# Kernel optimization log

Measured on AMD Instinct MI355X. Metric: run time of the kernel, lower is better.

The kernel has to match this reference:

```python
import jax, jax.numpy as jnp
import numpy as np

N_NODES = 100000
IN_CH, HIDDEN, OUT_CH = 128, 128, 64
N_POS, N_NEG = 600000, 600000


def _glorot(key, shape):
    lim = float(np.sqrt(6.0 / (shape[0] + shape[1])))
    return jax.random.uniform(key, shape, jnp.float32, -lim, lim)


def setup_inputs() -> dict:
    key = jax.random.key(0)
    k = jax.random.split(key, 7)
    x = jax.random.normal(k[0], (N_NODES, IN_CH), jnp.float32)
    pos_edge_index = jax.random.randint(k[1], (2, N_POS), 0, N_NODES, jnp.int64)
    neg_edge_index = jax.random.randint(k[2], (2, N_NEG), 0, N_NODES, jnp.int64)
    W1 = _glorot(k[3], (IN_CH, HIDDEN))
    b1 = jnp.zeros((HIDDEN,), jnp.float32)
    W2 = _glorot(k[4], (HIDDEN, OUT_CH))
    b2 = jnp.zeros((OUT_CH,), jnp.float32)
    return {"x": x, "pos_edge_index": pos_edge_index, "neg_edge_index": neg_edge_index,
            "W1": W1, "b1": b1, "W2": W2, "b2": b2}


def gcn_conv(x, W, b, src, dst, n_nodes):
    # PyG GCNConv: add self-loops, symmetric deg^-1/2 normalization, linear, bias
    h = x @ W                                               # [N, F_out]
    ones = jnp.ones(src.shape, h.dtype)
    deg = jax.ops.segment_sum(ones, dst, num_segments=n_nodes) + 1.0  # self-loop
    dinv = jax.lax.rsqrt(deg)                               # deg^-0.5, deg >= 1
    norm = dinv[src] * dinv[dst]                            # per-edge norm
    agg = jax.ops.segment_sum(h[src] * norm[:, None], dst, num_segments=n_nodes)
    agg = agg + h * (dinv * dinv)[:, None]                  # self-loop messages
    return agg + b


def reference(x, pos_edge_index, neg_edge_index, W1, b1, W2, b2):
    n = x.shape[0]
    src, dst = pos_edge_index[0], pos_edge_index[1]
    z = gcn_conv(x, W1, b1, src, dst, n)
    z = jax.nn.relu(z)
    z = gcn_conv(z, W2, b2, src, dst, n)
    # decode: gather endpoints of pos+neg edges, elementwise product, sum over feat
    ei = jnp.concatenate([pos_edge_index, neg_edge_index], axis=-1)  # [2, E_pos+E_neg]
    return jnp.sum(z[ei[0]] * z[ei[1]], axis=-1)
```

## Files before the change

### kernel.cpp

```cpp
#include <hip/hip_runtime.h>

#define N_NODES 100000
#define IN_CH 128
#define HIDDEN 128
#define OUT_CH 64
#define N_POS 600000
#define N_NEG 600000

typedef unsigned int uint32;
typedef unsigned short ushort16;
typedef __attribute__((ext_vector_type(8))) short bf16x8;
typedef __attribute__((ext_vector_type(4))) float f32x4;

__device__ inline float bf_lo(uint32 u) {
    union { uint32 i; float f; } v;
    v.i = u << 16;
    return v.f;
}
__device__ inline float bf_hi(uint32 u) {
    union { uint32 i; float f; } v;
    v.i = u & 0xffff0000u;
    return v.f;
}
__device__ inline ushort16 f2bf(float f) {
    union { uint32 i; float f; } v;
    v.f = f;
    uint32 r = v.i + 0x7fffu + ((v.i >> 16) & 1u);
    return (ushort16)(r >> 16);
}
__device__ inline uint32 pack2bf(float a, float b) {
    return (uint32)f2bf(a) | ((uint32)f2bf(b) << 16);
}

#define NB_HIST4 ((N_POS / 4 + 255) / 256)
#define NB_FILL4 ((N_POS / 4 + 255) / 256)
#define NB_GEMM1 ((N_NODES + 63) / 64)

__global__ void hist_wt(const int* __restrict__ dst, int* __restrict__ hist,
                        const float* __restrict__ W1, const float* __restrict__ W2,
                        ushort16* __restrict__ W1t, ushort16* __restrict__ W2t) {
    if (blockIdx.x < NB_HIST4) {
        int e = (blockIdx.x * 256 + threadIdx.x) * 4;
        if (e < N_POS) {
            int4 d4 = *(const int4*)(dst + e);
            atomicAdd(&hist[d4.x], 1);
            atomicAdd(&hist[d4.y], 1);
            atomicAdd(&hist[d4.z], 1);
            atomicAdd(&hist[d4.w], 1);
        }
    } else {
        int i = (blockIdx.x - NB_HIST4) * 256 + threadIdx.x;
        if (i < 128 * 128) {
            int n = i >> 7, k = i & 127;
            W1t[i] = f2bf(W1[k * 128 + n]);
        } else {
            int j = i - 128 * 128;
            if (j < 64 * 128) {
                int n = j >> 7, k = j & 127;
                W2t[j] = f2bf(W2[k * 64 + n]);
            }
        }
    }
}

__global__ void scan_reduce(const int* __restrict__ hist, int* __restrict__ partials, int n) {
    __shared__ int sdata[256];
    int b = blockIdx.x, t = threadIdx.x;
    int base = b * 1024;
    int s = 0;
    for (int i = t; i < 1024; i += 256) {
        int idx = base + i;
        s += (idx < n) ? hist[idx] : 0;
    }
    sdata[t] = s;
    __syncthreads();
    for (int off = 128; off > 0; off >>= 1) {
        if (t < off) sdata[t] += sdata[t + off];
        __syncthreads();
    }
    if (t == 0) partials[b] = sdata[0];
}

__global__ void scan_final(const int* __restrict__ hist, const int* __restrict__ partials,
                           int* __restrict__ rowstart, int* __restrict__ cursor,
                           float* __restrict__ dinv, int n) {
    __shared__ int tsum[256];
    __shared__ int base_sh;
    int t = threadIdx.x, b = blockIdx.x;
    if (t < 64) {
        int s0 = (t < b) ? partials[t] : 0;
        int i2 = t + 64;
        int s1 = (i2 < b && i2 < 98) ? partials[i2] : 0;
        int s = s0 + s1;
#pragma unroll
        for (int off = 32; off > 0; off >>= 1) s += __shfl_down(s, off, 64);
        if (t == 0) base_sh = s;
    }
    int base = b * 1024 + t * 4;
    int v[4];
    int s = 0;
#pragma unroll
    for (int j = 0; j < 4; j++) {
        int i = base + j;
        v[j] = (i < n) ? hist[i] : 0;
        s += v[j];
    }
    tsum[t] = s;
    __syncthreads();
    for (int off = 1; off < 256; off <<= 1) {
        int a = (t >= off) ? tsum[t - off] : 0;
        __syncthreads();
        tsum[t] += a;
        __syncthreads();
    }
    int offset = base_sh + (tsum[t] - s);
#pragma unroll
    for (int j = 0; j < 4; j++) {
        int i = base + j;
        if (i < n) {
            rowstart[i] = offset;
            cursor[i] = offset;
            dinv[i] = rsqrtf((float)v[j] + 1.0f);
            offset += v[j];
        }
    }
    if (b == 0 && t == 0) rowstart[n] = N_POS;
}

template <int M, bool XBF>
__device__ __forceinline__ void gemm_tile(const void* __restrict__ Xv,
                                          const ushort16* __restrict__ Wt,
                                          ushort16* __restrict__ H, int n, int tileIdx) {
    constexpr int K = 128;
    constexpr int TN = 64;
    constexpr int KH = 64;
    constexpr int XS = 72;
    __shared__ short Xs[TN * XS];
    __shared__ short Ws[M * XS];
    int tid = threadIdx.x;
    int node0 = tileIdx * TN;

    constexpr int CT = M / 16;
    int w = tid >> 6;
    int lane = tid & 63;
    int l15 = lane & 15;
    int quad = lane >> 4;
    f32x4 acc[CT] = {};

#pragma unroll
    for (int h = 0; h < 2; ++h) {
        if (h) __syncthreads();
        for (int q = tid; q < M * 8; q += 256) {
            int row = q >> 3, c = q & 7;
            uint4 v = *(const uint4*)((const short*)Wt + row * K + h * KH + c * 8);
            *(uint4*)(Ws + row * XS + c * 8) = v;
        }
        if (!XBF) {
            const float* X = (const float*)Xv;
            int row = tid >> 2, part = tid & 3;
            int gn = node0 + row;
#pragma unroll
            for (int c = 0; c < 4; ++c) {
                int kl = part * 16 + c * 4;
                float4 v = (gn < n) ? *(const float4*)(X + (size_t)gn * K + h * KH + kl)
                                    : float4{0, 0, 0, 0};
                uint2 p = {pack2bf(v.x, v.y), pack2bf(v.z, v.w)};
                *(uint2*)(Xs + row * XS + kl) = p;
            }
        } else {
            const short* X = (const short*)Xv;
            for (int q = tid; q < TN * 8; q += 256) {
                int row = q >> 3, c = q & 7;
                int gn = node0 + row;
                uint4 v = (gn < n) ? *(const uint4*)(X + (size_t)gn * K + h * KH + c * 8)
                                   : uint4{0, 0, 0, 0};
                *(uint4*)(Xs + row * XS + c * 8) = v;
            }
        }
        __syncthreads();

        const short* xrow = Xs + (w * 16 + l15) * XS + quad * 8;
#pragma unroll
        for (int kk = 0; kk < 2; ++kk) {
            bf16x8 a = *(const bf16x8*)(xrow + kk * 32);
#pragma unroll
            for (int ct = 0; ct < CT; ++ct) {
                bf16x8 b = *(const bf16x8*)(Ws + (ct * 16 + l15) * XS + quad * 8 + kk * 32);
                acc[ct] = __builtin_amdgcn_mfma_f32_16x16x32_bf16(a, b, acc[ct], 0, 0, 0);
            }
        }
    }

#pragma unroll
    for (int ct = 0; ct < CT; ++ct) {
#pragma unroll
        for (int r = 0; r < 4; ++r) {
            int gn = node0 + w * 16 + quad * 4 + r;
            if (gn < n) H[(size_t)gn * M + ct * 16 + l15] = f2bf(acc[ct][r]);
        }
    }
}

__global__ __launch_bounds__(256) void csr_gemm1(
    const int* __restrict__ src, const int* __restrict__ dst, const float* __restrict__ dinv,
    int* __restrict__ cursor, int2* __restrict__ adjw, const float* __restrict__ x,
    const ushort16* __restrict__ W1t, ushort16* __restrict__ H, int n) {
    if (blockIdx.x < NB_FILL4) {
        int e = (blockIdx.x * 256 + threadIdx.x) * 4;
        if (e < N_POS) {
            int4 s4 = *(const int4*)(src + e);
            int4 d4 = *(const int4*)(dst + e);
            float a0 = dinv[s4.x], a1 = dinv[s4.y], a2 = dinv[s4.z], a3 = dinv[s4.w];
            float c0 = dinv[d4.x], c1 = dinv[d4.y], c2 = dinv[d4.z], c3 = dinv[d4.w];
            int p0 = atomicAdd(&cursor[d4.x], 1);
            int p1 = atomicAdd(&cursor[d4.y], 1);
            int p2 = atomicAdd(&cursor[d4.z], 1);
            int p3 = atomicAdd(&cursor[d4.w], 1);
            adjw[p0] = int2{s4.x, __float_as_int(a0 * c0)};
            adjw[p1] = int2{s4.y, __float_as_int(a1 * c1)};
            adjw[p2] = int2{s4.z, __float_as_int(a2 * c2)};
            adjw[p3] = int2{s4.w, __float_as_int(a3 * c3)};
        }
    } else {
        gemm_tile<HIDDEN, false>(x, W1t, H, n, blockIdx.x - NB_FILL4);
    }
}

__device__ __forceinline__ uint4 agg_node128(int node, int l, const int* __restrict__ rowstart,
                                             const int2* __restrict__ adjw,
                                             const float* __restrict__ dinv,
                                             const ushort16* __restrict__ H,
                                             const float* __restrict__ bias) {
    float dn = dinv[node];
    int rs = rowstart[node], re = rowstart[node + 1];
    int deg = re - rs;
    int pc = (deg > 0) ? rs : (rs > 0 ? rs - 1 : 0);
    uint4 h[8];
    float wv[8];
#pragma unroll
    for (int j = 0; j < 8; ++j) {
        int p = (rs + j < re) ? rs + j : pc;
        int2 e = adjw[p];
        h[j] = *(const uint4*)(H + (size_t)e.x * 128 + l * 8);
        wv[j] = (j < deg) ? __int_as_float(e.y) : 0.0f;
    }
    float s0[8] = {}, s1[8] = {};
#pragma unroll
    for (int j = 0; j < 8; j += 2) {
        s0[0] += bf_lo(h[j].x) * wv[j]; s0[1] += bf_hi(h[j].x) * wv[j];
        s0[2] += bf_lo(h[j].y) * wv[j]; s0[3] += bf_hi(h[j].y) * wv[j];
        s0[4] += bf_lo(h[j].z) * wv[j]; s0[5] += bf_hi(h[j].z) * wv[j];
        s0[6] += bf_lo(h[j].w) * wv[j]; s0[7] += bf_hi(h[j].w) * wv[j];
        s1[0] += bf_lo(h[j + 1].x) * wv[j + 1]; s1[1] += bf_hi(h[j + 1].x) * wv[j + 1];
        s1[2] += bf_lo(h[j + 1].y) * wv[j + 1]; s1[3] += bf_hi(h[j + 1].y) * wv[j + 1];
        s1[4] += bf_lo(h[j + 1].z) * wv[j + 1]; s1[5] += bf_hi(h[j + 1].z) * wv[j + 1];
        s1[6] += bf_lo(h[j + 1].w) * wv[j + 1]; s1[7] += bf_hi(h[j + 1].w) * wv[j + 1];
    }
    for (int p = rs + 8; p < re; ++p) {
        int2 e = adjw[p];
        float w = __int_as_float(e.y);
        uint4 hh = *(const uint4*)(H + (size_t)e.x * 128 + l * 8);
        s0[0] += bf_lo(hh.x) * w; s0[1] += bf_hi(hh.x) * w;
        s0[2] += bf_lo(hh.y) * w; s0[3] += bf_hi(hh.y) * w;
        s0[4] += bf_lo(hh.z) * w; s0[5] += bf_hi(hh.z) * w;
        s0[6] += bf_lo(hh.w) * w; s0[7] += bf_hi(hh.w) * w;
    }
    uint4 hv = *(const uint4*)(H + (size_t)node * 128 + l * 8);
    float4 bv0 = *(const float4*)(bias + l * 8);
    float4 bv1 = *(const float4*)(bias + l * 8 + 4);
    float d2 = dn * dn;
    float hs[8] = {bf_lo(hv.x), bf_hi(hv.x), bf_lo(hv.y), bf_hi(hv.y),
                   bf_lo(hv.z), bf_hi(hv.z), bf_lo(hv.w), bf_hi(hv.w)};
    float bb[8] = {bv0.x, bv0.y, bv0.z, bv0.w, bv1.x, bv1.y, bv1.z, bv1.w};
    float v[8];
#pragma unroll
    for (int j = 0; j < 8; ++j) {
        v[j] = fmaxf(s0[j] + s1[j] + hs[j] * d2 + bb[j], 0.0f);
    }
    return uint4{pack2bf(v[0], v[1]), pack2bf(v[2], v[3]), pack2bf(v[4], v[5]),
                 pack2bf(v[6], v[7])};
}

#define ZS 136
__global__ __launch_bounds__(256, 4) void agg1_gemm2(
    const int* __restrict__ rowstart, const int2* __restrict__ adjw,
    const float* __restrict__ dinv, const ushort16* __restrict__ H,
    const float* __restrict__ b1, const ushort16* __restrict__ W2t,
    ushort16* __restrict__ h2, int n) {
    __shared__ __align__(16) short Zs[64 * ZS];
    __shared__ __align__(16) short Ws[64 * ZS];
    int tid = threadIdx.x;
    int node0 = blockIdx.x * 64;

    for (int q = tid; q < 64 * 16; q += 256) {
        int row = q >> 4, c = q & 15;
        uint4 v = *(const uint4*)((const short*)W2t + row * 128 + c * 8);
        *(uint4*)(Ws + row * ZS + c * 8) = v;
    }

    int g = tid >> 4, l = tid & 15;
#pragma unroll 1
    for (int it = 0; it < 4; ++it) {
        int row = g * 4 + it;
        int node = node0 + row;
        uint4 z = (node < n) ? agg_node128(node, l, rowstart, adjw, dinv, H, b1)
                             : uint4{0, 0, 0, 0};
        *(uint4*)(Zs + row * ZS + l * 8) = z;
    }
    __syncthreads();

    int w = tid >> 6, lane = tid & 63, l15 = lane & 15, quad = lane >> 4;
    f32x4 acc[4] = {};
    const short* zrow = Zs + (w * 16 + l15) * ZS + quad * 8;
#pragma unroll
    for (int kk = 0; kk < 4; ++kk) {
        bf16x8 a = *(const bf16x8*)(zrow + kk * 32);
#pragma unroll
        for (int ct = 0; ct < 4; ++ct) {
            bf16x8 b = *(const bf16x8*)(Ws + (ct * 16 + l15) * ZS + quad * 8 + kk * 32);
            acc[ct] = __builtin_amdgcn_mfma_f32_16x16x32_bf16(a, b, acc[ct], 0, 0, 0);
        }
    }
#pragma unroll
    for (int ct = 0; ct < 4; ++ct) {
#pragma unroll
        for (int r = 0; r < 4; ++r) {
            int gn = node0 + w * 16 + quad * 4 + r;
            if (gn < n) h2[(size_t)gn * OUT_CH + ct * 16 + l15] = f2bf(acc[ct][r]);
        }
    }
}

template <int F, bool RELU>
__global__ void agg_pull(const int* __restrict__ rowstart, const int2* __restrict__ adjw,
                         const float* __restrict__ dinv, const ushort16* __restrict__ H,
                         const float* __restrict__ bias, ushort16* __restrict__ Z, int n) {
    int g = threadIdx.x >> 4;
    int l = threadIdx.x & 15;
    int node = blockIdx.x * (blockDim.x >> 4) + g;
    if (node >= n) return;
    float dn = dinv[node];
    int rs = rowstart[node], re = rowstart[node + 1];
    int deg = re - rs;
    int pc = (deg > 0) ? rs : (rs > 0 ? rs - 1 : 0);
    if (F == 128) {
        uint4 h[8];
        float wv[8];
#pragma unroll
        for (int j = 0; j < 8; ++j) {
            int p = (rs + j < re) ? rs + j : pc;
            int2 e = adjw[p];
            h[j] = *(const uint4*)(H + (size_t)e.x * F + l * 8);
            wv[j] = (j < deg) ? __int_as_float(e.y) : 0.0f;
        }
        float s0[8] = {}, s1[8] = {};
#pragma unroll
        for (int j = 0; j < 8; j += 2) {
            s0[0] += bf_lo(h[j].x) * wv[j]; s0[1] += bf_hi(h[j].x) * wv[j];
            s0[2] += bf_lo(h[j].y) * wv[j]; s0[3] += bf_hi(h[j].y) * wv[j];
            s0[4] += bf_lo(h[j].z) * wv[j]; s0[5] += bf_hi(h[j].z) * wv[j];
            s0[6] += bf_lo(h[j].w) * wv[j]; s0[7] += bf_hi(h[j].w) * wv[j];
            s1[0] += bf_lo(h[j + 1].x) * wv[j + 1]; s1[1] += bf_hi(h[j + 1].x) * wv[j + 1];
            s1[2] += bf_lo(h[j + 1].y) * wv[j + 1]; s1[3] += bf_hi(h[j + 1].y) * wv[j + 1];
            s1[4] += bf_lo(h[j + 1].z) * wv[j + 1]; s1[5] += bf_hi(h[j + 1].z) * wv[j + 1];
            s1[6] += bf_lo(h[j + 1].w) * wv[j + 1]; s1[7] += bf_hi(h[j + 1].w) * wv[j + 1];
        }
        for (int p = rs + 8; p < re; ++p) {
            int2 e = adjw[p];
            float w = __int_as_float(e.y);
            uint4 hh = *(const uint4*)(H + (size_t)e.x * F + l * 8);
            s0[0] += bf_lo(hh.x) * w; s0[1] += bf_hi(hh.x) * w;
            s0[2] += bf_lo(hh.y) * w; s0[3] += bf_hi(hh.y) * w;
            s0[4] += bf_lo(hh.z) * w; s0[5] += bf_hi(hh.z) * w;
            s0[6] += bf_lo(hh.w) * w; s0[7] += bf_hi(hh.w) * w;
        }
        uint4 hv = *(const uint4*)(H + (size_t)node * F + l * 8);
        float4 bv0 = *(const float4*)(bias + l * 8);
        float4 bv1 = *(const float4*)(bias + l * 8 + 4);
        float d2 = dn * dn;
        float hs[8] = {bf_lo(hv.x), bf_hi(hv.x), bf_lo(hv.y), bf_hi(hv.y),
                       bf_lo(hv.z), bf_hi(hv.z), bf_lo(hv.w), bf_hi(hv.w)};
        float bb[8] = {bv0.x, bv0.y, bv0.z, bv0.w, bv1.x, bv1.y, bv1.z, bv1.w};
        float v[8];
#pragma unroll
        for (int j = 0; j < 8; ++j) {
            v[j] = s0[j] + s1[j] + hs[j] * d2 + bb[j];
            if (RELU) v[j] = fmaxf(v[j], 0.0f);
        }
        *(uint4*)(Z + (size_t)node * F + l * 8) =
            uint4{pack2bf(v[0], v[1]), pack2bf(v[2], v[3]), pack2bf(v[4], v[5]),
                  pack2bf(v[6], v[7])};
    } else {
        uint2 h[8];
        float wv[8];
#pragma unroll
        for (int j = 0; j < 8; ++j) {
            int p = (rs + j < re) ? rs + j : pc;
            int2 e = adjw[p];
            h[j] = *(const uint2*)(H + (size_t)e.x * F + l * 4);
            wv[j] = (j < deg) ? __int_as_float(e.y) : 0.0f;
        }
        float s0[4] = {}, s1[4] = {};
#pragma unroll
        for (int j = 0; j < 8; j += 2) {
            s0[0] += bf_lo(h[j].x) * wv[j]; s0[1] += bf_hi(h[j].x) * wv[j];
            s0[2] += bf_lo(h[j].y) * wv[j]; s0[3] += bf_hi(h[j].y) * wv[j];
            s1[0] += bf_lo(h[j + 1].x) * wv[j + 1]; s1[1] += bf_hi(h[j + 1].x) * wv[j + 1];
            s1[2] += bf_lo(h[j + 1].y) * wv[j + 1]; s1[3] += bf_hi(h[j + 1].y) * wv[j + 1];
        }
        for (int p = rs + 8; p < re; ++p) {
            int2 e = adjw[p];
            float w = __int_as_float(e.y);
            uint2 hh = *(const uint2*)(H + (size_t)e.x * F + l * 4);
            s0[0] += bf_lo(hh.x) * w; s0[1] += bf_hi(hh.x) * w;
            s0[2] += bf_lo(hh.y) * w; s0[3] += bf_hi(hh.y) * w;
        }
        uint2 hv = *(const uint2*)(H + (size_t)node * F + l * 4);
        float4 bv = *(const float4*)(bias + l * 4);
        float d2 = dn * dn;
        float hs[4] = {bf_lo(hv.x), bf_hi(hv.x), bf_lo(hv.y), bf_hi(hv.y)};
        float bb[4] = {bv.x, bv.y, bv.z, bv.w};
        float v[4];
#pragma unroll
        for (int j = 0; j < 4; ++j) {
            v[j] = s0[j] + s1[j] + hs[j] * d2 + bb[j];
            if (RELU) v[j] = fmaxf(v[j], 0.0f);
        }
        *(uint2*)(Z + (size_t)node * F + l * 4) = uint2{pack2bf(v[0], v[1]), pack2bf(v[2], v[3])};
    }
}

__global__ void decode_mfma(const int* __restrict__ pos, const int* __restrict__ neg,
                            const short* __restrict__ Z, float* __restrict__ out) {
    int wid = threadIdx.x >> 6;
    int lane = threadIdx.x & 63;
    int l15 = lane & 15;
    int quad = lane >> 4;
    int e0 = (blockIdx.x * 4 + wid) * 32;
    if (e0 >= N_POS + N_NEG) return;
    const int* bp = (e0 < N_POS) ? pos : (neg - N_POS);
    int eA = e0 + l15;
    int eB = e0 + 16 + l15;
    int aA = bp[eA], bA = bp[600000 + eA];
    int aB = bp[eB], bB = bp[600000 + eB];

    const short* zaA = Z + (size_t)aA * OUT_CH + quad * 8;
    const short* zbA = Z + (size_t)bA * OUT_CH + quad * 8;
    const short* zaB = Z + (size_t)aB * OUT_CH + quad * 8;
    const short* zbB = Z + (size_t)bB * OUT_CH + quad * 8;
    bf16x8 a0A = *(const bf16x8*)(zaA);
    bf16x8 a1A = *(const bf16x8*)(zaA + 32);
    bf16x8 b0A = *(const bf16x8*)(zbA);
    bf16x8 b1A = *(const bf16x8*)(zbA + 32);
    bf16x8 a0B = *(const bf16x8*)(zaB);
    bf16x8 a1B = *(const bf16x8*)(zaB + 32);
    bf16x8 b0B = *(const bf16x8*)(zbB);
    bf16x8 b1B = *(const bf16x8*)(zbB + 32);

    f32x4 accA = {}, accB = {};
    accA = __builtin_amdgcn_mfma_f32_16x16x32_bf16(a0A, b0A, accA, 0, 0, 0);
    accB = __builtin_amdgcn_mfma_f32_16x16x32_bf16(a0B, b0B, accB, 0, 0, 0);
    accA = __builtin_amdgcn_mfma_f32_16x16x32_bf16(a1A, b1A, accA, 0, 0, 0);
    accB = __builtin_amdgcn_mfma_f32_16x16x32_bf16(a1B, b1B, accB, 0, 0, 0);

    if (quad == (l15 >> 2)) {
        out[eA] = accA[l15 & 3];
        out[eB] = accB[l15 & 3];
    }
}

extern "C" void kernel_launch(void* const* d_in, const int* in_sizes, int n_in,
                              void* d_out, int out_size, void* d_ws, size_t ws_size,
                              hipStream_t stream) {
    const float* x = (const float*)d_in[0];
    const int* pos = (const int*)d_in[1];
    const int* neg = (const int*)d_in[2];
    const float* W1 = (const float*)d_in[3];
    const float* b1 = (const float*)d_in[4];
    const float* W2 = (const float*)d_in[5];
    const float* b2 = (const float*)d_in[6];
    float* out = (float*)d_out;

    ushort16* A = (ushort16*)d_ws;
    ushort16* B = A + (size_t)N_NODES * 128;
    float* dinv = (float*)(B + (size_t)N_NODES * 128);
    int* hist = (int*)(dinv + N_NODES);
    int* rowstart = hist + N_NODES;
    int* cursor = rowstart + N_NODES + 1;
    int2* adjw = (int2*)(cursor + N_NODES);
    int* partials = (int*)(adjw + N_POS);
    ushort16* W1t = (ushort16*)(partials + 128);
    ushort16* W2t = W1t + 128 * 128;

    const int* pos_src = pos;
    const int* pos_dst = pos + N_POS;

    constexpr int NB_SCAN = (N_NODES + 1023) / 1024;

    hipMemsetAsync(hist, 0, N_NODES * sizeof(int), stream);
    hist_wt<<<NB_HIST4 + 96, 256, 0, stream>>>(pos_dst, hist, W1, W2, W1t, W2t);
    scan_reduce<<<NB_SCAN, 256, 0, stream>>>(hist, partials, N_NODES);
    scan_final<<<NB_SCAN, 256, 0, stream>>>(hist, partials, rowstart, cursor, dinv, N_NODES);

    csr_gemm1<<<NB_FILL4 + NB_GEMM1, 256, 0, stream>>>(pos_src, pos_dst, dinv, cursor, adjw, x,
                                                       W1t, A, N_NODES);

    agg1_gemm2<<<(N_NODES + 63) / 64, 256, 0, stream>>>(rowstart, adjw, dinv, A, b1, W2t, B,
                                                        N_NODES);

    agg_pull<OUT_CH, false><<<(N_NODES + 15) / 16, 256, 0, stream>>>(rowstart, adjw, dinv, B, b2,
                                                                     A, N_NODES);

    decode_mfma<<<(N_POS + N_NEG) / 128, 256, 0, stream>>>(pos, neg, (const short*)A, out);
}
```

Baseline: 275.9 us.

## Fold symmetric normalization into GEMM epilogues and drop per-edge weights from CSR

Pre-scales GEMM outputs by dinv[src] so aggregation becomes an unweighted sum followed by a single multiply by dinv[dst]. The CSR adjacency shrinks from int2 (src, weight) to plain int src. This removes the dinv gathers in the fill kernel and halves adjacency traffic in both aggregation passes. Padded neighbor slots now read an extra zero row at index N_NODES, written by the GEMM epilogue through the gn<=n guard. The histogram and fill kernels are also changed back from four edges per thread to one edge per thread.

```diff
diff --git a/kernel.cpp b/kernel.cpp
--- a/kernel.cpp
+++ b/kernel.cpp
@@ -32,24 +32,18 @@
     return (uint32)f2bf(a) | ((uint32)f2bf(b) << 16);
 }
 
-#define NB_HIST4 ((N_POS / 4 + 255) / 256)
-#define NB_FILL4 ((N_POS / 4 + 255) / 256)
+#define NB_HIST ((N_POS + 255) / 256)
+#define NB_FILL ((N_POS + 255) / 256)
 #define NB_GEMM1 ((N_NODES + 63) / 64)
 
 __global__ void hist_wt(const int* __restrict__ dst, int* __restrict__ hist,
                         const float* __restrict__ W1, const float* __restrict__ W2,
                         ushort16* __restrict__ W1t, ushort16* __restrict__ W2t) {
-    if (blockIdx.x < NB_HIST4) {
-        int e = (blockIdx.x * 256 + threadIdx.x) * 4;
-        if (e < N_POS) {
-            int4 d4 = *(const int4*)(dst + e);
-            atomicAdd(&hist[d4.x], 1);
-            atomicAdd(&hist[d4.y], 1);
-            atomicAdd(&hist[d4.z], 1);
-            atomicAdd(&hist[d4.w], 1);
-        }
+    if (blockIdx.x < NB_HIST) {
+        int i = blockIdx.x * 256 + threadIdx.x;
+        if (i < N_POS) atomicAdd(&hist[dst[i]], 1);
     } else {
-        int i = (blockIdx.x - NB_HIST4) * 256 + threadIdx.x;
+        int i = (blockIdx.x - NB_HIST) * 256 + threadIdx.x;
         if (i < 128 * 128) {
             int n = i >> 7, k = i & 127;
             W1t[i] = f2bf(W1[k * 128 + n]);
@@ -127,9 +121,10 @@
     if (b == 0 && t == 0) rowstart[n] = N_POS;
 }
 
-template <int M, bool XBF>
+template <int M, bool XBF, bool SCALE>
 __device__ __forceinline__ void gemm_tile(const void* __restrict__ Xv,
                                           const ushort16* __restrict__ Wt,
+                                          const float* __restrict__ dinv,
                                           ushort16* __restrict__ H, int n, int tileIdx) {
     constexpr int K = 128;
     constexpr int TN = 64;
@@ -191,43 +186,40 @@
         }
     }
 
+    float sc[4];
+#pragma unroll
+    for (int r = 0; r < 4; ++r) {
+        int gn = node0 + w * 16 + quad * 4 + r;
+        sc[r] = SCALE ? ((gn < n) ? dinv[gn] : 0.0f) : 1.0f;
+    }
 #pragma unroll
     for (int ct = 0; ct < CT; ++ct) {
 #pragma unroll
         for (int r = 0; r < 4; ++r) {
             int gn = node0 + w * 16 + quad * 4 + r;
-            if (gn < n) H[(size_t)gn * M + ct * 16 + l15] = f2bf(acc[ct][r]);
+            if (gn <= n) H[(size_t)gn * M + ct * 16 + l15] = f2bf(acc[ct][r] * sc[r]);
         }
     }
 }
 
 __global__ __launch_bounds__(256) void csr_gemm1(
     const int* __restrict__ src, const int* __restrict__ dst, const float* __restrict__ dinv,
-    int* __restrict__ cursor, int2* __restrict__ adjw, const float* __restrict__ x,
+    int* __restrict__ cursor, int* __restrict__ adj, const float* __restrict__ x,
     const ushort16* __restrict__ W1t, ushort16* __restrict__ H, int n) {
-    if (blockIdx.x < NB_FILL4) {
-        int e = (blockIdx.x * 256 + threadIdx.x) * 4;
+    if (blockIdx.x < NB_FILL) {
+        int e = blockIdx.x * 256 + threadIdx.x;
         if (e < N_POS) {
-            int4 s4 = *(const int4*)(src + e);
-            int4 d4 = *(const int4*)(dst + e);
-            float a0 = dinv[s4.x], a1 = dinv[s4.y], a2 = dinv[s4.z], a3 = dinv[s4.w];
-            float c0 = dinv[d4.x], c1 = dinv[d4.y], c2 = dinv[d4.z], c3 = dinv[d4.w];
-            int p0 = atomicAdd(&cursor[d4.x], 1);
-            int p1 = atomicAdd(&cursor[d4.y], 1);
-            int p2 = atomicAdd(&cursor[d4.z], 1);
-            int p3 = atomicAdd(&cursor[d4.w], 1);
-            adjw[p0] = int2{s4.x, __float_as_int(a0 * c0)};
-            adjw[p1] = int2{s4.y, __float_as_int(a1 * c1)};
-            adjw[p2] = int2{s4.z, __float_as_int(a2 * c2)};
-            adjw[p3] = int2{s4.w, __float_as_int(a3 * c3)};
+            int s = src[e], d = dst[e];
+            int p = atomicAdd(&cursor[d], 1);
+            adj[p] = s;
         }
     } else {
-        gemm_tile<HIDDEN, false>(x, W1t, H, n, blockIdx.x - NB_FILL4);
+        gemm_tile<HIDDEN, false, true>(x, W1t, dinv, H, n, blockIdx.x - NB_FILL);
     }
 }
 
 __device__ __forceinline__ uint4 agg_node128(int node, int l, const int* __restrict__ rowstart,
-                                             const int2* __restrict__ adjw,
+                                             const int* __restrict__ adj,
                                              const float* __restrict__ dinv,
                                              const ushort16* __restrict__ H,
                                              const float* __restrict__ bias) {
@@ -236,46 +228,43 @@
     int deg = re - rs;
     int pc = (deg > 0) ? rs : (rs > 0 ? rs - 1 : 0);
     uint4 h[8];
-    float wv[8];
 #pragma unroll
     for (int j = 0; j < 8; ++j) {
         int p = (rs + j < re) ? rs + j : pc;
-        int2 e = adjw[p];
-        h[j] = *(const uint4*)(H + (size_t)e.x * 128 + l * 8);
-        wv[j] = (j < deg) ? __int_as_float(e.y) : 0.0f;
+        int s = adj[p];
+        int idx = (j < deg) ? s : N_NODES;
+        h[j] = *(const uint4*)(H + (size_t)idx * 128 + l * 8);
     }
     float s0[8] = {}, s1[8] = {};
 #pragma unroll
     for (int j = 0; j < 8; j += 2) {
-        s0[0] += bf_lo(h[j].x) * wv[j]; s0[1] += bf_hi(h[j].x) * wv[j];
-        s0[2] += bf_lo(h[j].y) * wv[j]; s0[3] += bf_hi(h[j].y) * wv[j];
-        s0[4] += bf_lo(h[j].z) * wv[j]; s0[5] += bf_hi(h[j].z) * wv[j];
-        s0[6] += bf_lo(h[j].w) * wv[j]; s0[7] += bf_hi(h[j].w) * wv[j];
-        s1[0] += bf_lo(h[j + 1].x) * wv[j + 1]; s1[1] += bf_hi(h[j + 1].x) * wv[j + 1];
-        s1[2] += bf_lo(h[j + 1].y) * wv[j + 1]; s1[3] += bf_hi(h[j + 1].y) * wv[j + 1];
-        s1[4] += bf_lo(h[j + 1].z) * wv[j + 1]; s1[5] += bf_hi(h[j + 1].z) * wv[j + 1];
-        s1[6] += bf_lo(h[j + 1].w) * wv[j + 1]; s1[7] += bf_hi(h[j + 1].w) * wv[j + 1];
+        s0[0] += bf_lo(h[j].x); s0[1] += bf_hi(h[j].x);
+        s0[2] += bf_lo(h[j].y); s0[3] += bf_hi(h[j].y);
+        s0[4] += bf_lo(h[j].z); s0[5] += bf_hi(h[j].z);
+        s0[6] += bf_lo(h[j].w); s0[7] += bf_hi(h[j].w);
+        s1[0] += bf_lo(h[j + 1].x); s1[1] += bf_hi(h[j + 1].x);
+        s1[2] += bf_lo(h[j + 1].y); s1[3] += bf_hi(h[j + 1].y);
+        s1[4] += bf_lo(h[j + 1].z); s1[5] += bf_hi(h[j + 1].z);
+        s1[6] += bf_lo(h[j + 1].w); s1[7] += bf_hi(h[j + 1].w);
     }
     for (int p = rs + 8; p < re; ++p) {
-        int2 e = adjw[p];
-        float w = __int_as_float(e.y);
-        uint4 hh = *(const uint4*)(H + (size_t)e.x * 128 + l * 8);
-        s0[0] += bf_lo(hh.x) * w; s0[1] += bf_hi(hh.x) * w;
-        s0[2] += bf_lo(hh.y) * w; s0[3] += bf_hi(hh.y) * w;
-        s0[4] += bf_lo(hh.z) * w; s0[5] += bf_hi(hh.z) * w;
-        s0[6] += bf_lo(hh.w) * w; s0[7] += bf_hi(hh.w) * w;
+        int idx = adj[p];
+        uint4 hh = *(const uint4*)(H + (size_t)idx * 128 + l * 8);
+        s0[0] += bf_lo(hh.x); s0[1] += bf_hi(hh.x);
+        s0[2] += bf_lo(hh.y); s0[3] += bf_hi(hh.y);
+        s0[4] += bf_lo(hh.z); s0[5] += bf_hi(hh.z);
+        s0[6] += bf_lo(hh.w); s0[7] += bf_hi(hh.w);
     }
     uint4 hv = *(const uint4*)(H + (size_t)node * 128 + l * 8);
     float4 bv0 = *(const float4*)(bias + l * 8);
     float4 bv1 = *(const float4*)(bias + l * 8 + 4);
-    float d2 = dn * dn;
     float hs[8] = {bf_lo(hv.x), bf_hi(hv.x), bf_lo(hv.y), bf_hi(hv.y),
                    bf_lo(hv.z), bf_hi(hv.z), bf_lo(hv.w), bf_hi(hv.w)};
     float bb[8] = {bv0.x, bv0.y, bv0.z, bv0.w, bv1.x, bv1.y, bv1.z, bv1.w};
     float v[8];
 #pragma unroll
     for (int j = 0; j < 8; ++j) {
-        v[j] = fmaxf(s0[j] + s1[j] + hs[j] * d2 + bb[j], 0.0f);
+        v[j] = fmaxf((s0[j] + s1[j] + hs[j]) * dn + bb[j], 0.0f);
     }
     return uint4{pack2bf(v[0], v[1]), pack2bf(v[2], v[3]), pack2bf(v[4], v[5]),
                  pack2bf(v[6], v[7])};
@@ -283,7 +272,7 @@
 
 #define ZS 136
 __global__ __launch_bounds__(256, 4) void agg1_gemm2(
-    const int* __restrict__ rowstart, const int2* __restrict__ adjw,
+    const int* __restrict__ rowstart, const int* __restrict__ adj,
     const float* __restrict__ dinv, const ushort16* __restrict__ H,
     const float* __restrict__ b1, const ushort16* __restrict__ W2t,
     ushort16* __restrict__ h2, int n) {
@@ -303,7 +292,7 @@
     for (int it = 0; it < 4; ++it) {
         int row = g * 4 + it;
         int node = node0 + row;
-        uint4 z = (node < n) ? agg_node128(node, l, rowstart, adjw, dinv, H, b1)
+        uint4 z = (node < n) ? agg_node128(node, l, rowstart, adj, dinv, H, b1)
                              : uint4{0, 0, 0, 0};
         *(uint4*)(Zs + row * ZS + l * 8) = z;
     }
@@ -321,18 +310,24 @@
             acc[ct] = __builtin_amdgcn_mfma_f32_16x16x32_bf16(a, b, acc[ct], 0, 0, 0);
         }
     }
+    float sc[4];
+#pragma unroll
+    for (int r = 0; r < 4; ++r) {
+        int gn = node0 + w * 16 + quad * 4 + r;
+        sc[r] = (gn < n) ? dinv[gn] : 0.0f;
+    }
 #pragma unroll
     for (int ct = 0; ct < 4; ++ct) {
 #pragma unroll
         for (int r = 0; r < 4; ++r) {
             int gn = node0 + w * 16 + quad * 4 + r;
-            if (gn < n) h2[(size_t)gn * OUT_CH + ct * 16 + l15] = f2bf(acc[ct][r]);
+            if (gn <= n) h2[(size_t)gn * OUT_CH + ct * 16 + l15] = f2bf(acc[ct][r] * sc[r]);
         }
     }
 }
 
 template <int F, bool RELU>
-__global__ void agg_pull(const int* __restrict__ rowstart, const int2* __restrict__ adjw,
+__global__ void agg_pull(const int* __restrict__ rowstart, const int* __restrict__ adj,
                          const float* __restrict__ dinv, const ushort16* __restrict__ H,
                          const float* __restrict__ bias, ushort16* __restrict__ Z, int n) {
     int g = threadIdx.x >> 4;
@@ -345,46 +340,43 @@
     int pc = (deg > 0) ? rs : (rs > 0 ? rs - 1 : 0);
     if (F == 128) {
         uint4 h[8];
-        float wv[8];
 #pragma unroll
         for (int j = 0; j < 8; ++j) {
             int p = (rs + j < re) ? rs + j : pc;
-            int2 e = adjw[p];
-            h[j] = *(const uint4*)(H + (size_t)e.x * F + l * 8);
-            wv[j] = (j < deg) ? __int_as_float(e.y) : 0.0f;
+            int s = adj[p];
+            int idx = (j < deg) ? s : N_NODES;
+            h[j] = *(const uint4*)(H + (size_t)idx * F + l * 8);
         }
         float s0[8] = {}, s1[8] = {};
 #pragma unroll
         for (int j = 0; j < 8; j += 2) {
-            s0[0] += bf_lo(h[j].x) * wv[j]; s0[1] += bf_hi(h[j].x) * wv[j];
-            s0[2] += bf_lo(h[j].y) * wv[j]; s0[3] += bf_hi(h[j].y) * wv[j];
-            s0[4] += bf_lo(h[j].z) * wv[j]; s0[5] += bf_hi(h[j].z) * wv[j];
-            s0[6] += bf_lo(h[j].w) * wv[j]; s0[7] += bf_hi(h[j].w) * wv[j];
-            s1[0] += bf_lo(h[j + 1].x) * wv[j + 1]; s1[1] += bf_hi(h[j + 1].x) * wv[j + 1];
-            s1[2] += bf_lo(h[j + 1].y) * wv[j + 1]; s1[3] += bf_hi(h[j + 1].y) * wv[j + 1];
-            s1[4] += bf_lo(h[j + 1].z) * wv[j + 1]; s1[5] += bf_hi(h[j + 1].z) * wv[j + 1];
-            s1[6] += bf_lo(h[j + 1].w) * wv[j + 1]; s1[7] += bf_hi(h[j + 1].w) * wv[j + 1];
+            s0[0] += bf_lo(h[j].x); s0[1] += bf_hi(h[j].x);
+            s0[2] += bf_lo(h[j].y); s0[3] += bf_hi(h[j].y);
+            s0[4] += bf_lo(h[j].z); s0[5] += bf_hi(h[j].z);
+            s0[6] += bf_lo(h[j].w); s0[7] += bf_hi(h[j].w);
+            s1[0] += bf_lo(h[j + 1].x); s1[1] += bf_hi(h[j + 1].x);
+            s1[2] += bf_lo(h[j + 1].y); s1[3] += bf_hi(h[j + 1].y);
+            s1[4] += bf_lo(h[j + 1].z); s1[5] += bf_hi(h[j + 1].z);
+            s1[6] += bf_lo(h[j + 1].w); s1[7] += bf_hi(h[j + 1].w);
         }
         for (int p = rs + 8; p < re; ++p) {
-            int2 e = adjw[p];
-            float w = __int_as_float(e.y);
-            uint4 hh = *(const uint4*)(H + (size_t)e.x * F + l * 8);
-            s0[0] += bf_lo(hh.x) * w; s0[1] += bf_hi(hh.x) * w;
-            s0[2] += bf_lo(hh.y) * w; s0[3] += bf_hi(hh.y) * w;
-            s0[4] += bf_lo(hh.z) * w; s0[5] += bf_hi(hh.z) * w;
-            s0[6] += bf_lo(hh.w) * w; s0[7] += bf_hi(hh.w) * w;
+            int idx = adj[p];
+            uint4 hh = *(const uint4*)(H + (size_t)idx * F + l * 8);
+            s0[0] += bf_lo(hh.x); s0[1] += bf_hi(hh.x);
+            s0[2] += bf_lo(hh.y); s0[3] += bf_hi(hh.y);
+            s0[4] += bf_lo(hh.z); s0[5] += bf_hi(hh.z);
+            s0[6] += bf_lo(hh.w); s0[7] += bf_hi(hh.w);
         }
         uint4 hv = *(const uint4*)(H + (size_t)node * F + l * 8);
         float4 bv0 = *(const float4*)(bias + l * 8);
         float4 bv1 = *(const float4*)(bias + l * 8 + 4);
-        float d2 = dn * dn;
         float hs[8] = {bf_lo(hv.x), bf_hi(hv.x), bf_lo(hv.y), bf_hi(hv.y),
                        bf_lo(hv.z), bf_hi(hv.z), bf_lo(hv.w), bf_hi(hv.w)};
         float bb[8] = {bv0.x, bv0.y, bv0.z, bv0.w, bv1.x, bv1.y, bv1.z, bv1.w};
         float v[8];
 #pragma unroll
         for (int j = 0; j < 8; ++j) {
-            v[j] = s0[j] + s1[j] + hs[j] * d2 + bb[j];
+            v[j] = (s0[j] + s1[j] + hs[j]) * dn + bb[j];
             if (RELU) v[j] = fmaxf(v[j], 0.0f);
         }
         *(uint4*)(Z + (size_t)node * F + l * 8) =
@@ -392,38 +384,35 @@
                   pack2bf(v[6], v[7])};
     } else {
         uint2 h[8];
-        float wv[8];
 #pragma unroll
         for (int j = 0; j < 8; ++j) {
             int p = (rs + j < re) ? rs + j : pc;
-            int2 e = adjw[p];
-            h[j] = *(const uint2*)(H + (size_t)e.x * F + l * 4);
-            wv[j] = (j < deg) ? __int_as_float(e.y) : 0.0f;
+            int s = adj[p];
+            int idx = (j < deg) ? s : N_NODES;
+            h[j] = *(const uint2*)(H + (size_t)idx * F + l * 4);
         }
         float s0[4] = {}, s1[4] = {};
 #pragma unroll
         for (int j = 0; j < 8; j += 2) {
-            s0[0] += bf_lo(h[j].x) * wv[j]; s0[1] += bf_hi(h[j].x) * wv[j];
-            s0[2] += bf_lo(h[j].y) * wv[j]; s0[3] += bf_hi(h[j].y) * wv[j];
-            s1[0] += bf_lo(h[j + 1].x) * wv[j + 1]; s1[1] += bf_hi(h[j + 1].x) * wv[j + 1];
-            s1[2] += bf_lo(h[j + 1].y) * wv[j + 1]; s1[3] += bf_hi(h[j + 1].y) * wv[j + 1];
+            s0[0] += bf_lo(h[j].x); s0[1] += bf_hi(h[j].x);
+            s0[2] += bf_lo(h[j].y); s0[3] += bf_hi(h[j].y);
+            s1[0] += bf_lo(h[j + 1].x); s1[1] += bf_hi(h[j + 1].x);
+            s1[2] += bf_lo(h[j + 1].y); s1[3] += bf_hi(h[j + 1].y);
         }
         for (int p = rs + 8; p < re; ++p) {
-            int2 e = adjw[p];
-            float w = __int_as_float(e.y);
-            uint2 hh = *(const uint2*)(H + (size_t)e.x * F + l * 4);
-            s0[0] += bf_lo(hh.x) * w; s0[1] += bf_hi(hh.x) * w;
-            s0[2] += bf_lo(hh.y) * w; s0[3] += bf_hi(hh.y) * w;
+            int idx = adj[p];
+            uint2 hh = *(const uint2*)(H + (size_t)idx * F + l * 4);
+            s0[0] += bf_lo(hh.x); s0[1] += bf_hi(hh.x);
+            s0[2] += bf_lo(hh.y); s0[3] += bf_hi(hh.y);
         }
         uint2 hv = *(const uint2*)(H + (size_t)node * F + l * 4);
         float4 bv = *(const float4*)(bias + l * 4);
-        float d2 = dn * dn;
         float hs[4] = {bf_lo(hv.x), bf_hi(hv.x), bf_lo(hv.y), bf_hi(hv.y)};
         float bb[4] = {bv.x, bv.y, bv.z, bv.w};
         float v[4];
 #pragma unroll
         for (int j = 0; j < 4; ++j) {
-            v[j] = s0[j] + s1[j] + hs[j] * d2 + bb[j];
+            v[j] = (s0[j] + s1[j] + hs[j]) * dn + bb[j];
             if (RELU) v[j] = fmaxf(v[j], 0.0f);
         }
         *(uint2*)(Z + (size_t)node * F + l * 4) = uint2{pack2bf(v[0], v[1]), pack2bf(v[2], v[3])};
@@ -482,13 +471,13 @@
     float* out = (float*)d_out;
 
     ushort16* A = (ushort16*)d_ws;
-    ushort16* B = A + (size_t)N_NODES * 128;
-    float* dinv = (float*)(B + (size_t)N_NODES * 128);
+    ushort16* B = A + (size_t)(N_NODES + 1) * 128;
+    float* dinv = (float*)(B + (size_t)(N_NODES + 1) * 64);
     int* hist = (int*)(dinv + N_NODES);
     int* rowstart = hist + N_NODES;
     int* cursor = rowstart + N_NODES + 1;
-    int2* adjw = (int2*)(cursor + N_NODES);
-    int* partials = (int*)(adjw + N_POS);
+    int* adj = cursor + N_NODES;
+    int* partials = adj + N_POS;
     ushort16* W1t = (ushort16*)(partials + 128);
     ushort16* W2t = W1t + 128 * 128;
 
@@ -498,17 +487,17 @@
     constexpr int NB_SCAN = (N_NODES + 1023) / 1024;
 
     hipMemsetAsync(hist, 0, N_NODES * sizeof(int), stream);
-    hist_wt<<<NB_HIST4 + 96, 256, 0, stream>>>(pos_dst, hist, W1, W2, W1t, W2t);
+    hist_wt<<<NB_HIST + 96, 256, 0, stream>>>(pos_dst, hist, W1, W2, W1t, W2t);
     scan_reduce<<<NB_SCAN, 256, 0, stream>>>(hist, partials, N_NODES);
     scan_final<<<NB_SCAN, 256, 0, stream>>>(hist, partials, rowstart, cursor, dinv, N_NODES);
 
-    csr_gemm1<<<NB_FILL4 + NB_GEMM1, 256, 0, stream>>>(pos_src, pos_dst, dinv, cursor, adjw, x,
-                                                       W1t, A, N_NODES);
-
-    agg1_gemm2<<<(N_NODES + 63) / 64, 256, 0, stream>>>(rowstart, adjw, dinv, A, b1, W2t, B,
+    csr_gemm1<<<NB_FILL + NB_GEMM1, 256, 0, stream>>>(pos_src, pos_dst, dinv, cursor, adj, x,
+                                                      W1t, A, N_NODES);
+
+    agg1_gemm2<<<(N_NODES + 63) / 64, 256, 0, stream>>>(rowstart, adj, dinv, A, b1, W2t, B,
                                                         N_NODES);
 
-    agg_pull<OUT_CH, false><<<(N_NODES + 15) / 16, 256, 0, stream>>>(rowstart, adjw, dinv, B, b2,
+    agg_pull<OUT_CH, false><<<(N_NODES + 15) / 16, 256, 0, stream>>>(rowstart, adj, dinv, B, b2,
                                                                      A, N_NODES);
 
     decode_mfma<<<(N_POS + N_NEG) / 128, 256, 0, stream>>>(pos, neg, (const short*)A, out);
```

New measurement: 302.3 us. +9.6%, slower.
